# Kernel optimization log

Hardware: AMD Instinct MI355X
Metric: run time of the kernel (lower is better)

Reference implementation:

```python
import jax, jax.numpy as jnp
import numpy as np

NODE_F = 8      # node_features
HID = 128       # hidden_dim
HEADS = 8       # nn.MultiheadAttention num_heads
OUT = 256       # output_dim
MAX_ATOMS = 4096  # max_pocket_atoms
NEIGHBOR_RADIUS = 3.0   # _compute_surface_scores neighbor_radius


def setup_inputs() -> dict:
    key = jax.random.key(0)
    ks = jax.random.split(key, 16)
    N, M = 16384, 32
    x = jax.random.normal(ks[0], (N, NODE_F), dtype=jnp.float32)
    pos = jax.random.normal(ks[1], (N, 3), dtype=jnp.float32) * 10.0
    ligand_pos = jax.random.normal(ks[2], (M, 3), dtype=jnp.float32) * 3.0

    def lin(k, fan_in, fan_out):
        return jax.random.normal(k, (fan_in, fan_out), dtype=jnp.float32) / np.sqrt(fan_in)

    return {
        'x': x, 'pos': pos, 'ligand_pos': ligand_pos,
        'W_node': lin(ks[3], NODE_F, HID), 'b_node': jnp.zeros((HID,), jnp.float32),
        'Wq': lin(ks[4], HID, HID), 'bq': jnp.zeros((HID,), jnp.float32),
        'Wk': lin(ks[5], HID, HID), 'bk': jnp.zeros((HID,), jnp.float32),
        'Wv': lin(ks[6], HID, HID), 'bv': jnp.zeros((HID,), jnp.float32),
        'Wo': lin(ks[7], HID, HID), 'bo': jnp.zeros((HID,), jnp.float32),
        'W1': lin(ks[8], HID, OUT), 'b1': jnp.zeros((OUT,), jnp.float32),
        'W2': lin(ks[9], OUT, OUT), 'b2': jnp.zeros((OUT,), jnp.float32),
    }


def _select_binding_site(pos, ligand_pos, k):
    # select_by_binding_site_proximity: distance-to-ligand-center + surface scores, topk
    lig_center = jnp.mean(ligand_pos, axis=0)                       # [3]
    d_lig = jnp.linalg.norm(pos - lig_center, axis=1)               # [N]
    # _compute_surface_scores: cdist(pos,pos) < 3.0, count neighbors (minus self)
    sq = jnp.sum(pos * pos, axis=1)                                 # [N]
    d2 = sq[:, None] + sq[None, :] - 2.0 * (pos @ pos.T)            # [N,N] squared distances
    neighbor_counts = jnp.sum(d2 < NEIGHBOR_RADIUS ** 2, axis=1) - 1
    surface = 1.0 / (neighbor_counts.astype(jnp.float32) + 1.0)
    scores = 1.0 / (1.0 + d_lig / 5.0) + 0.5 * surface
    _, idx = jax.lax.top_k(scores, k)                               # largest=True
    return idx


def reference(x, pos, ligand_pos, W_node, b_node, Wq, bq, Wk, bk, Wv, bv, Wo, bo, W1, b1, W2, b2):
    # N > max_pocket_atoms -> smart selection (adaptive with ligand_pos => binding_site)
    idx = _select_binding_site(pos, ligand_pos, MAX_ATOMS)
    xs = x[idx]                                                     # [K, NODE_F]

    # node embedding (E3 net call fails in the original -> h = node_embedding(x))
    h = xs @ W_node + b_node                                        # [K, HID]

    # MultiheadAttention over the single (batch=None) sequence, eval mode (no dropout)
    K = MAX_ATOMS
    dh = HID // HEADS
    q = (h @ Wq + bq).reshape(K, HEADS, dh).transpose(1, 0, 2)      # [H,K,dh]
    k_ = (h @ Wk + bk).reshape(K, HEADS, dh).transpose(1, 0, 2)
    v = (h @ Wv + bv).reshape(K, HEADS, dh).transpose(1, 0, 2)
    attn = jax.nn.softmax(jnp.einsum('hqd,hkd->hqk', q, k_) / np.sqrt(dh), axis=-1)
    av = jnp.einsum('hqk,hkd->hqd', attn, v).transpose(1, 0, 2).reshape(K, HID)
    h_att = av @ Wo + bo                                            # [K, HID]

    # global mean pool + output projection (Linear-ReLU-Linear)
    pooled = jnp.mean(h_att, axis=0)                                # [HID]
    out = jax.nn.relu(pooled @ W1 + b1) @ W2 + b2                   # [OUT]
    return out
```

## Files before the change

### kernel.cpp

```cpp
#include <hip/hip_runtime.h>
#include <cstdint>
#include <cstddef>

#define NPTS 16384
#define KSEL 4096
#define HIDDEN 128
#define NHEADS 8
#define DHEAD 16
#define OUTD 256
#define NSLICE 4
#define FCAP 262144
#define LCAP 2048
#define TAU 0.15f
#define HROW 264

typedef __attribute__((ext_vector_type(8))) short bf16x8;
typedef __attribute__((ext_vector_type(4))) float f32x4;
typedef __attribute__((ext_vector_type(16))) float f32x16;

#if defined(__has_builtin)
#if __has_builtin(__builtin_amdgcn_exp2f)
#define E2(x) __builtin_amdgcn_exp2f(x)
#endif
#endif
#ifndef E2
#define E2(x) exp2f(x)
#endif

constexpr size_t OFF_PA    = 1024;
constexpr size_t OFF_PB    = OFF_PA  + (size_t)NPTS*32;
constexpr size_t OFF_SQ    = OFF_PB  + (size_t)NPTS*32;
constexpr size_t OFF_DL    = OFF_SQ  + (size_t)NPTS*4;
constexpr size_t OFF_CNT   = OFF_DL  + (size_t)NPTS*4;
constexpr size_t OFF_NFLAG = OFF_CNT + (size_t)NPTS*4;
constexpr size_t OFF_FLG   = OFF_NFLAG + 1024;
constexpr size_t OFF_SEL   = OFF_FLG + (size_t)FCAP*4;
constexpr size_t SZ_PK     = (size_t)NHEADS*KSEL*32*2;
constexpr size_t OFF_QPK   = OFF_SEL + (size_t)KSEL*4;
constexpr size_t OFF_KPK   = OFF_QPK + SZ_PK;
constexpr size_t OFF_V     = OFF_KPK + SZ_PK;
constexpr size_t OFF_LP    = OFF_V  + (size_t)KSEL*HIDDEN*4;
constexpr size_t OFF_WP    = OFF_LP + (size_t)NHEADS*KSEL*NSLICE*4;
constexpr size_t OFF_PAV   = OFF_WP + (size_t)NHEADS*KSEL*NSLICE*4;
constexpr size_t OFF_WSP   = OFF_PAV + 1024;

__device__ __forceinline__ unsigned short f2bf(float f) {
    union { float f; unsigned u; } v; v.f = f;
    unsigned r = v.u + 0x7fffu + ((v.u >> 16) & 1u);
    return (unsigned short)(r >> 16);
}
__device__ __forceinline__ float bf2f(unsigned short h) {
    union { unsigned u; float f; } v; v.u = ((unsigned)h) << 16;
    return v.f;
}

__global__ void __launch_bounds__(256) k_prep(const float* __restrict__ pos, const float* __restrict__ lig, int M,
                       unsigned short* __restrict__ pa, unsigned short* __restrict__ pb,
                       float* __restrict__ sq, float* __restrict__ dl,
                       int* __restrict__ cnt, unsigned int* __restrict__ nflag, float* __restrict__ pav) {
    __shared__ float ls[128];
    __shared__ float ctr[3];
    int tid = threadIdx.x;
    int i = blockIdx.x * 256 + tid;
    cnt[i] = 0;
    if (i == 0) *nflag = 0;
    if (blockIdx.x == 0 && tid < HIDDEN) pav[tid] = 0.f;
    for (int k = tid; k < 3 * M; k += 256) ls[k] = lig[k];
    __syncthreads();
    if (tid < 3) {
        float s = 0.f;
        for (int k = 0; k < M; k++) s += ls[k * 3 + tid];
        ctr[tid] = s / (float)M;
    }
    __syncthreads();
    float x = pos[i*3+0], y = pos[i*3+1], z = pos[i*3+2];
    float s = (x*x + y*y) + z*z;
    sq[i] = s;
    float dx = x - ctr[0], dy = y - ctr[1], dz = z - ctr[2];
    dl[i] = sqrtf((dx*dx + dy*dy) + dz*dz);
    unsigned short xh = f2bf(x); float xr = bf2f(xh); float xl = x - xr;
    unsigned short yh = f2bf(y); float yr = bf2f(yh); float yl = y - yr;
    unsigned short zh = f2bf(z); float zr = bf2f(zh); float zl = z - zr;
    unsigned short xlb = f2bf(xl), ylb = f2bf(yl), zlb = f2bf(zl);
    unsigned short xhA = f2bf(-2.f*xr), xlA = f2bf(-2.f*xl);
    unsigned short yhA = f2bf(-2.f*yr), ylA = f2bf(-2.f*yl);
    unsigned short zhA = f2bf(-2.f*zr), zlA = f2bf(-2.f*zl);
    unsigned short sih = f2bf(s);
    unsigned short sil = f2bf(s - bf2f(sih));
    unsigned short one = f2bf(1.0f);
    union { unsigned short s[16]; float4 f[2]; } A, B;
    A.s[0]=xhA; A.s[1]=xhA; A.s[2]=xlA;
    A.s[3]=yhA; A.s[4]=yhA; A.s[5]=ylA;
    A.s[6]=zhA; A.s[7]=zhA; A.s[8]=zlA;
    A.s[9]=xlA; A.s[10]=ylA; A.s[11]=zlA;
    A.s[12]=sih; A.s[13]=sil; A.s[14]=one; A.s[15]=one;
    B.s[0]=xh;  B.s[1]=xlb;  B.s[2]=xh;
    B.s[3]=yh;  B.s[4]=ylb;  B.s[5]=yh;
    B.s[6]=zh;  B.s[7]=zlb;  B.s[8]=zh;
    B.s[9]=xlb; B.s[10]=ylb; B.s[11]=zlb;
    B.s[12]=one; B.s[13]=one; B.s[14]=sih; B.s[15]=sil;
    float4* pad = (float4*)(pa + (size_t)i * 16);
    pad[0] = A.f[0]; pad[1] = A.f[1];
    float4* pbd = (float4*)(pb + (size_t)i * 16);
    pbd[0] = B.f[0]; pbd[1] = B.f[1];
}

__global__ void __launch_bounds__(256) k_wsplit(const float* __restrict__ Wq, const float* __restrict__ Wk,
                                                const float* __restrict__ Wv, unsigned short* __restrict__ wsp) {
    const float* W = (blockIdx.x == 0) ? Wq : ((blockIdx.x == 1) ? Wk : Wv);
    unsigned short* dst = wsp + (size_t)blockIdx.x * HIDDEN * 256;
    for (int idx = threadIdx.x; idx < HIDDEN * HIDDEN; idx += 256) {
        int k = idx >> 7, n = idx & 127;
        float w = W[k * HIDDEN + n];
        unsigned short hi = f2bf(w);
        unsigned short lo = f2bf(w - bf2f(hi));
        dst[(size_t)n * 256 + k] = hi;
        dst[(size_t)n * 256 + 128 + k] = lo;
    }
}

__global__ void __launch_bounds__(256) k_neighbor(
        const unsigned short* __restrict__ pa, const unsigned short* __restrict__ pb,
        int* __restrict__ cnt, unsigned int* __restrict__ flg, unsigned int* __restrict__ nflag) {
    __shared__ unsigned short js[256 * 24];
    __shared__ unsigned int fbuf[LCAP];
    __shared__ unsigned int fcnt, fbase;
    int tid = threadIdx.x;
    if (tid == 0) fcnt = 0;
    int lane = tid & 63, w = tid >> 6;
    int half = lane >> 5, il = lane & 31;
    int i = blockIdx.x * 128 + w * 32 + il;
    bf16x8 bfrag = *(const bf16x8*)(pb + (size_t)i * 16 + half * 8);
    int jb0 = blockIdx.y * 1024;
    int acc = 0;
    for (int chv = 0; chv < 4; chv++) {
        int jb = jb0 + chv * 256;
        __syncthreads();
        {
            const float4* src = (const float4*)(pa + (size_t)(jb + tid) * 16);
            float4 v0 = src[0], v1 = src[1];
            float4* dst = (float4*)&js[tid * 24];
            dst[0] = v0; dst[1] = v1;
        }
        __syncthreads();
        #pragma unroll 2
        for (int t = 0; t < 8; t++) {
            bf16x8 afrag = *(const bf16x8*)&js[(t * 32 + il) * 24 + half * 8];
            f32x16 c = {0.f,0.f,0.f,0.f,0.f,0.f,0.f,0.f,0.f,0.f,0.f,0.f,0.f,0.f,0.f,0.f};
            c = __builtin_amdgcn_mfma_f32_32x32x16_bf16(afrag, bfrag, c, 0, 0, 0);
            int cs = 0, cl = 0;
            #pragma unroll
            for (int r = 0; r < 16; r++) {
                cs += (c[r] < 9.0f - TAU);
                cl += (c[r] < 9.0f + TAU);
            }
            if (cl == cs) {
                acc += cs;
            } else {
                unsigned jt9 = (unsigned)((jb >> 5) + t);
                unsigned xx = atomicAdd(&fcnt, 1u);
                if (xx < LCAP) fbuf[xx] = ((unsigned)i << 10) | (jt9 << 1) | (unsigned)half;
            }
        }
    }
    acc += __shfl_xor(acc, 32);
    if (half == 0) atomicAdd(&cnt[i], acc);
    __syncthreads();
    if (tid == 0) {
        unsigned cf = fcnt; if (cf > LCAP) cf = LCAP;
        fcnt = cf;
        fbase = atomicAdd(nflag, cf);
    }
    __syncthreads();
    unsigned cf = fcnt, fb = fbase;
    for (unsigned xx = tid; xx < cf; xx += 256) {
        unsigned di = fb + xx;
        if (di < FCAP) flg[di] = fbuf[xx];
    }
}

__global__ void __launch_bounds__(256) k_fixup(const float* __restrict__ pos, const float* __restrict__ sq,
        const unsigned int* __restrict__ flg, const unsigned int* __restrict__ nflag,
        int* __restrict__ cnt) {
    int nf = (int)*nflag; if (nf > FCAP) nf = FCAP;
    for (int idx = blockIdx.x * 256 + threadIdx.x; idx < nf; idx += gridDim.x * 256) {
        unsigned pr = flg[idx];
        int i = (int)(pr >> 10);
        int jt = (int)((pr >> 1) & 511u) << 5;
        int half = (int)(pr & 1u);
        float xi = pos[i*3+0], yi = pos[i*3+1], zi = pos[i*3+2];
        float si = sq[i];
        int add = 0;
        #pragma unroll
        for (int r = 0; r < 16; r++) {
            int j = jt + (r & 3) + 8 * (r >> 2) + 4 * half;
            float xj = pos[j*3+0], yj = pos[j*3+1], zj = pos[j*3+2];
            float dot = fmaf(xi, xj, fmaf(yi, yj, zi * zj));
            float d2 = (si + sq[j]) - 2.0f * dot;
            add += (d2 < 9.0f);
        }
        atomicAdd(&cnt[i], add);
    }
}

__global__ void __launch_bounds__(1024) k_select(const float* __restrict__ dl, const int* __restrict__ cnt,
                                                 int* __restrict__ sel) {
    __shared__ unsigned int sk[NPTS];
    __shared__ int hist[256];
    __shared__ int scan2[256];
    __shared__ unsigned int s_prefix;
    __shared__ int s_rem, s_eqtot, s_nout, s_digit, s_cgt;
    int tid = threadIdx.x;
    for (int i = tid; i < NPTS; i += 1024) {
        float score = 1.0f / (1.0f + dl[i] / 5.0f) + 0.5f * (1.0f / (float)cnt[i]);
        unsigned int u = __float_as_uint(score);
        sk[i] = u ^ ((u & 0x80000000u) ? 0xFFFFFFFFu : 0x80000000u);
    }
    if (tid == 0) { s_prefix = 0; s_rem = KSEL; s_nout = 0; s_eqtot = 0; }
    __syncthreads();
    for (int p = 0; p < 4; p++) {
        int sh = 24 - 8 * p;
        if (tid < 256) hist[tid] = 0;
        __syncthreads();
        unsigned int pref = s_prefix;
        int shp = (p == 0) ? 0 : (32 - 8 * p);
        for (int i = tid; i < NPTS; i += 1024) {
            unsigned int key = sk[i];
            bool m = (p == 0) || ((key >> shp) == pref);
            if (m) atomicAdd(&hist[(key >> sh) & 255], 1);
        }
        __syncthreads();
        if (tid < 256) scan2[tid] = hist[tid];
        __syncthreads();
        for (int off = 1; off < 256; off <<= 1) {
            int v = 0;
            if (tid < 256) { v = scan2[tid]; if (tid + off < 256) v += scan2[tid + off]; }
            __syncthreads();
            if (tid < 256) scan2[tid] = v;
            __syncthreads();
        }
        int rem = s_rem;
        if (tid < 256) {
            int hi = scan2[tid];
            int lo = hi - hist[tid];
            if (hi >= rem && lo < rem) { s_digit = tid; s_cgt = lo; }
        }
        __syncthreads();
        if (tid == 0) {
            s_prefix = (s_prefix << 8) | (unsigned int)s_digit;
            s_rem = rem - s_cgt;
            if (p == 3) s_eqtot = hist[s_digit];
        }
        __syncthreads();
    }
    unsigned int T = s_prefix;
    int need_eq = s_rem;
    for (int i = tid; i < NPTS; i += 1024)
        if (sk[i] > T) sel[atomicAdd(&s_nout, 1)] = i;
    __syncthreads();
    if (s_eqtot == need_eq) {
        for (int i = tid; i < NPTS; i += 1024)
            if (sk[i] == T) sel[atomicAdd(&s_nout, 1)] = i;
    } else {
        for (int i = tid; i < NPTS; i += 1024) {
            if (sk[i] == T) {
                int rank = 0;
                for (int j = 0; j < i; j++) rank += (sk[j] == T);
                if (rank < need_eq) sel[atomicAdd(&s_nout, 1)] = i;
            }
        }
    }
}

__global__ void __launch_bounds__(256) k_qkv(const float* __restrict__ x, const int* __restrict__ sel,
        const float* __restrict__ Wn, const float* __restrict__ bn,
        const float* __restrict__ bq, const float* __restrict__ bk, const float* __restrict__ bv,
        const unsigned short* __restrict__ wsp,
        unsigned short* __restrict__ qpk, unsigned short* __restrict__ kpk,
        float* __restrict__ vg) {
    __shared__ float xs[32][8];
    __shared__ unsigned short hsp[32 * HROW];
    int tid = threadIdx.x;
    int r0 = blockIdx.x * 32;
    int proj = blockIdx.y;
    { int rr = tid >> 3, cc = tid & 7; xs[rr][cc] = x[(size_t)sel[r0 + rr] * 8 + cc]; }
    __syncthreads();
    {
        int d = tid & 127, rp = tid >> 7;
        float wn[8];
        #pragma unroll
        for (int c = 0; c < 8; c++) wn[c] = Wn[c * HIDDEN + d];
        float b = bn[d];
        for (int r = rp; r < 32; r += 2) {
            float a = b;
            #pragma unroll
            for (int c = 0; c < 8; c++) a = fmaf(xs[r][c], wn[c], a);
            unsigned short hi = f2bf(a);
            unsigned short lo = f2bf(a - bf2f(hi));
            hsp[r * HROW + d] = hi;
            hsp[r * HROW + 128 + d] = lo;
        }
    }
    __syncthreads();
    int lane = tid & 63, w = tid >> 6;
    int n = lane & 15, g = lane >> 4;
    int rloc = (w & 1) * 16;
    int chalf = w >> 1;
    const unsigned short* wb = wsp + (size_t)proj * HIDDEN * 256;
    const unsigned short* arow = &hsp[(rloc + n) * HROW + ((g < 2) ? 0 : 128) + (g & 1) * 8];
    int b1off = (g & 1) * 8;
    for (int tc = 0; tc < 4; tc++) {
        int col0 = chalf * 64 + tc * 16;
        const unsigned short* bcol = wb + (size_t)(col0 + n) * 256;
        f32x4 acc = {0.f, 0.f, 0.f, 0.f};
        #pragma unroll
        for (int c = 0; c < 8; c++) {
            bf16x8 af = *(const bf16x8*)(arow + c * 16);
            bf16x8 b1 = *(const bf16x8*)(bcol + c * 16 + b1off);
            bf16x8 b2 = {0,0,0,0,0,0,0,0};
            if (g < 2) b2 = *(const bf16x8*)(bcol + 128 + c * 16 + b1off);
            acc = __builtin_amdgcn_mfma_f32_16x16x32_bf16(af, b1, acc, 0, 0, 0);
            acc = __builtin_amdgcn_mfma_f32_16x16x32_bf16(af, b2, acc, 0, 0, 0);
        }
        int col = col0 + n;
        int hh = col >> 4, dd = col & 15;
        if (proj == 0) {
            float bb = bq[col];
            #pragma unroll
            for (int r = 0; r < 4; r++) {
                int qrow = r0 + rloc + g * 4 + r;
                float val = (acc[r] + bb) * 0.36067376022224085f;
                unsigned short hi = f2bf(val);
                unsigned short lo = f2bf(val - bf2f(hi));
                size_t idx = ((size_t)(hh * KSEL) + qrow) * 32 + dd;
                qpk[idx] = hi; qpk[idx + 16] = lo;
            }
        } else if (proj == 1) {
            float bb = bk[col];
            #pragma unroll
            for (int r = 0; r < 4; r++) {
                int qrow = r0 + rloc + g * 4 + r;
                float val = acc[r] + bb;
                unsigned short hi = f2bf(val);
                unsigned short lo = f2bf(val - bf2f(hi));
                size_t idx = ((size_t)(hh * KSEL) + qrow) * 32 + dd;
                kpk[idx] = hi; kpk[idx + 16] = lo;
            }
        } else {
            float bb = bv[col];
            #pragma unroll
            for (int r = 0; r < 4; r++) {
                int qrow = r0 + rloc + g * 4 + r;
                vg[(size_t)qrow * HIDDEN + col] = acc[r] + bb;
            }
        }
    }
}

__global__ void __launch_bounds__(256) k_attn_l(
        const unsigned short* __restrict__ qpk, const unsigned short* __restrict__ kpk,
        float* __restrict__ lp) {
    __shared__ unsigned short smem[256 * 40];
    int tid = threadIdx.x;
    int ks = blockIdx.x, yg = blockIdx.y, h = blockIdx.z;
    size_t hb = (size_t)h * KSEL;
    int lane = tid & 63, w = tid >> 6;
    int n = lane & 15, g = lane >> 4;
    int q0w = yg * 64 + w * 16;
    bf16x8 afrag = *(const bf16x8*)(qpk + (hb + q0w + n) * 32 + g * 8);
    float l0 = 0.f, l1 = 0.f, l2 = 0.f, l3 = 0.f;
    int b1off = (g & 1) * 8;
    int b2off = 16 + g * 8;
    for (int kc = 0; kc < 4; kc++) {
        __syncthreads();
        {
            int krow = ks * 1024 + kc * 256 + tid;
            const float4* src = (const float4*)(kpk + (hb + krow) * 32);
            float4 a0 = src[0], a1 = src[1], a2 = src[2], a3 = src[3];
            float4* dst = (float4*)&smem[tid * 40];
            dst[0] = a0; dst[1] = a1; dst[2] = a2; dst[3] = a3;
        }
        __syncthreads();
        #pragma unroll 4
        for (int t = 0; t < 16; t++) {
            const unsigned short* rowp = &smem[(t * 16 + n) * 40];
            bf16x8 b1 = *(const bf16x8*)(rowp + b1off);
            bf16x8 b2 = {0,0,0,0,0,0,0,0};
            if (g < 2) b2 = *(const bf16x8*)(rowp + b2off);
            f32x4 c = {0.f, 0.f, 0.f, 0.f};
            c = __builtin_amdgcn_mfma_f32_16x16x32_bf16(afrag, b1, c, 0, 0, 0);
            c = __builtin_amdgcn_mfma_f32_16x16x32_bf16(afrag, b2, c, 0, 0, 0);
            l0 += E2(c[0]); l1 += E2(c[1]); l2 += E2(c[2]); l3 += E2(c[3]);
        }
    }
    #pragma unroll
    for (int m = 1; m < 16; m <<= 1) {
        l0 += __shfl_xor(l0, m); l1 += __shfl_xor(l1, m);
        l2 += __shfl_xor(l2, m); l3 += __shfl_xor(l3, m);
    }
    if (n == 0) {
        size_t base = (hb + q0w + g * 4) * NSLICE + ks;
        lp[base]            = l0; lp[base + NSLICE]     = l1;
        lp[base + 2*NSLICE] = l2; lp[base + 3*NSLICE]   = l3;
    }
}

__global__ void __launch_bounds__(256) k_attn_w(
        const unsigned short* __restrict__ qpk, const unsigned short* __restrict__ kpk,
        const float* __restrict__ lp, float* __restrict__ wp) {
    __shared__ unsigned short smem[256 * 40];
    __shared__ float rls[256];
    int tid = threadIdx.x;
    int qs = blockIdx.x, yg = blockIdx.y, h = blockIdx.z;
    size_t hb = (size_t)h * KSEL;
    int lane = tid & 63, w = tid >> 6;
    int n = lane & 15, g = lane >> 4;
    int j0w = yg * 64 + w * 16;
    bf16x8 afrag = *(const bf16x8*)(kpk + (hb + j0w + n) * 32 + g * 8);
    float w0 = 0.f, w1 = 0.f, w2 = 0.f, w3 = 0.f;
    int b1off = (g & 1) * 8;
    int b2off = 16 + g * 8;
    for (int qc = 0; qc < 4; qc++) {
        __syncthreads();
        {
            int qrow = qs * 1024 + qc * 256 + tid;
            const float4* src = (const float4*)(qpk + (hb + qrow) * 32);
            float4 a0 = src[0], a1 = src[1], a2 = src[2], a3 = src[3];
            float4* dst = (float4*)&smem[tid * 40];
            dst[0] = a0; dst[1] = a1; dst[2] = a2; dst[3] = a3;
            float4 p = ((const float4*)lp)[hb + qrow];
            rls[tid] = 1.0f / ((p.x + p.y) + (p.z + p.w));
        }
        __syncthreads();
        #pragma unroll 4
        for (int t = 0; t < 16; t++) {
            const unsigned short* rowp = &smem[(t * 16 + n) * 40];
            bf16x8 b1 = *(const bf16x8*)(rowp + b1off);
            bf16x8 b2 = {0,0,0,0,0,0,0,0};
            if (g < 2) b2 = *(const bf16x8*)(rowp + b2off);
            f32x4 c = {0.f, 0.f, 0.f, 0.f};
            c = __builtin_amdgcn_mfma_f32_16x16x32_bf16(afrag, b1, c, 0, 0, 0);
            c = __builtin_amdgcn_mfma_f32_16x16x32_bf16(afrag, b2, c, 0, 0, 0);
            float rv = rls[t * 16 + n];
            w0 = fmaf(E2(c[0]), rv, w0); w1 = fmaf(E2(c[1]), rv, w1);
            w2 = fmaf(E2(c[2]), rv, w2); w3 = fmaf(E2(c[3]), rv, w3);
        }
    }
    #pragma unroll
    for (int m = 1; m < 16; m <<= 1) {
        w0 += __shfl_xor(w0, m); w1 += __shfl_xor(w1, m);
        w2 += __shfl_xor(w2, m); w3 += __shfl_xor(w3, m);
    }
    if (n == 0) {
        size_t base = (hb + j0w + g * 4) * NSLICE + qs;
        wp[base]            = w0; wp[base + NSLICE]     = w1;
        wp[base + 2*NSLICE] = w2; wp[base + 3*NSLICE]   = w3;
    }
}

__global__ void __launch_bounds__(256) k_colsum(const float* __restrict__ wp, const float* __restrict__ vg,
                                                float* __restrict__ pav) {
    __shared__ float wl[NHEADS][32];
    __shared__ float red[128];
    int tid = threadIdx.x;
    int j0 = blockIdx.x * 32;
    {
        int h = tid >> 5, jl = tid & 31;
        float4 p = ((const float4*)wp)[(size_t)h * KSEL + j0 + jl];
        wl[h][jl] = (p.x + p.y) + (p.z + p.w);
    }
    __syncthreads();
    int d = tid & 127, g = tid >> 7;
    int h = d >> 4;
    float acc = 0.f;
    for (int jl = g * 16; jl < g * 16 + 16; jl++)
        acc = fmaf(wl[h][jl], vg[(size_t)(j0 + jl) * HIDDEN + d], acc);
    if (g == 1) red[d] = acc;
    __syncthreads();
    if (g == 0) atomicAdd(&pav[d], (acc + red[d]) * (1.0f / (float)KSEL));
}

__global__ void __launch_bounds__(256) k_final(const float* __restrict__ pav,
        const float* __restrict__ Wo, const float* __restrict__ bo,
        const float* __restrict__ W1, const float* __restrict__ b1,
        const float* __restrict__ W2, const float* __restrict__ b2,
        float* __restrict__ out) {
    __shared__ float sp[HIDDEN];
    __shared__ float st[OUTD];
    int t = threadIdx.x;
    if (t < HIDDEN) {
        float a = bo[t];
        for (int c = 0; c < HIDDEN; c++) a = fmaf(pav[c], Wo[c * HIDDEN + t], a);
        sp[t] = a;
    }
    __syncthreads();
    {
        float a = b1[t];
        for (int c = 0; c < HIDDEN; c++) a = fmaf(sp[c], W1[c * OUTD + t], a);
        st[t] = fmaxf(a, 0.f);
    }
    __syncthreads();
    {
        float o = b2[t];
        for (int c = 0; c < OUTD; c++) o = fmaf(st[c], W2[c * OUTD + t], o);
        out[t] = o;
    }
}

extern "C" void kernel_launch(void* const* d_in, const int* in_sizes, int n_in,
                              void* d_out, int out_size, void* d_ws, size_t ws_size,
                              hipStream_t stream) {
    (void)n_in; (void)out_size; (void)ws_size;
    const float* x   = (const float*)d_in[0];
    const float* pos = (const float*)d_in[1];
    const float* lig = (const float*)d_in[2];
    const float* Wn  = (const float*)d_in[3];
    const float* bn  = (const float*)d_in[4];
    const float* Wq  = (const float*)d_in[5];
    const float* bq  = (const float*)d_in[6];
    const float* Wk  = (const float*)d_in[7];
    const float* bk  = (const float*)d_in[8];
    const float* Wv  = (const float*)d_in[9];
    const float* bv  = (const float*)d_in[10];
    const float* Wo  = (const float*)d_in[11];
    const float* bo  = (const float*)d_in[12];
    const float* W1  = (const float*)d_in[13];
    const float* b1  = (const float*)d_in[14];
    const float* W2  = (const float*)d_in[15];
    const float* b2  = (const float*)d_in[16];
    int M = in_sizes[2] / 3;

    char* ws = (char*)d_ws;
    unsigned short* pa  = (unsigned short*)(ws + OFF_PA);
    unsigned short* pb  = (unsigned short*)(ws + OFF_PB);
    float*          sq  = (float*)(ws + OFF_SQ);
    float*          dl  = (float*)(ws + OFF_DL);
    int*            cnt = (int*)  (ws + OFF_CNT);
    unsigned int*   nfl = (unsigned int*)(ws + OFF_NFLAG);
    unsigned int*   flg = (unsigned int*)(ws + OFF_FLG);
    int*            sel = (int*)  (ws + OFF_SEL);
    unsigned short* qpk = (unsigned short*)(ws + OFF_QPK);
    unsigned short* kpk = (unsigned short*)(ws + OFF_KPK);
    float*          vg  = (float*)(ws + OFF_V);
    float*          lp  = (float*)(ws + OFF_LP);
    float*          wp  = (float*)(ws + OFF_WP);
    float*          pav = (float*)(ws + OFF_PAV);
    unsigned short* wsp = (unsigned short*)(ws + OFF_WSP);

    hipLaunchKernelGGL(k_prep,     dim3(64),       dim3(256),  0, stream, pos, lig, M, pa, pb, sq, dl, cnt, nfl, pav);
    hipLaunchKernelGGL(k_wsplit,   dim3(3),        dim3(256),  0, stream, Wq, Wk, Wv, wsp);
    hipLaunchKernelGGL(k_neighbor, dim3(128, 16),  dim3(256),  0, stream, pa, pb, cnt, flg, nfl);
    hipLaunchKernelGGL(k_fixup,    dim3(128),      dim3(256),  0, stream, pos, sq, flg, nfl, cnt);
    hipLaunchKernelGGL(k_select,   dim3(1),        dim3(1024), 0, stream, dl, cnt, sel);
    hipLaunchKernelGGL(k_qkv,      dim3(128, 3),   dim3(256),  0, stream, x, sel, Wn, bn, bq, bk, bv, wsp, qpk, kpk, vg);
    hipLaunchKernelGGL(k_attn_l,   dim3(4, 64, 8), dim3(256),  0, stream, qpk, kpk, lp);
    hipLaunchKernelGGL(k_attn_w,   dim3(4, 64, 8), dim3(256),  0, stream, qpk, kpk, lp, wp);
    hipLaunchKernelGGL(k_colsum,   dim3(KSEL/32),  dim3(256),  0, stream, wp, vg, pav);
    hipLaunchKernelGGL(k_final,    dim3(1),        dim3(256),  0, stream, pav, Wo, bo, W1, b1, W2, b2, (float*)d_out);
}
```

Before: 288.1 us.

## Use 32x32 MFMA tiles in attention kernels and fold weight split into prep

Both attention passes (softmax denominator and column-weight) switch from 16x16x32 MFMA tiles to 32x32x16 tiles, with each wave covering 32 rows. The three-term split-bf16 product (hi*hi + lo*hi + hi*lo) is computed explicitly, so the zero-padded fragment of the old layout goes away, the MFMA count per score drops and the grid is halved. The weight hi/lo split kernel is merged into k_prep as three extra blocks, removing one launch. In exchange each thread keeps 16 accumulators, which raises register pressure, and the cross-lane reductions and scattered stores grow.

Result: faster. 276.1 us (-4.2%).

```diff
diff --git a/kernel.cpp b/kernel.cpp
--- a/kernel.cpp
+++ b/kernel.cpp
@@ -57,10 +57,26 @@
 __global__ void __launch_bounds__(256) k_prep(const float* __restrict__ pos, const float* __restrict__ lig, int M,
                        unsigned short* __restrict__ pa, unsigned short* __restrict__ pb,
                        float* __restrict__ sq, float* __restrict__ dl,
-                       int* __restrict__ cnt, unsigned int* __restrict__ nflag, float* __restrict__ pav) {
+                       int* __restrict__ cnt, unsigned int* __restrict__ nflag, float* __restrict__ pav,
+                       const float* __restrict__ Wq, const float* __restrict__ Wk, const float* __restrict__ Wv,
+                       unsigned short* __restrict__ wsp) {
     __shared__ float ls[128];
     __shared__ float ctr[3];
     int tid = threadIdx.x;
+    if (blockIdx.x >= 64) {
+        int proj = blockIdx.x - 64;
+        const float* W = (proj == 0) ? Wq : ((proj == 1) ? Wk : Wv);
+        unsigned short* dst = wsp + (size_t)proj * HIDDEN * 256;
+        for (int idx = tid; idx < HIDDEN * HIDDEN; idx += 256) {
+            int k = idx >> 7, n = idx & 127;
+            float w = W[k * HIDDEN + n];
+            unsigned short hi = f2bf(w);
+            unsigned short lo = f2bf(w - bf2f(hi));
+            dst[(size_t)n * 256 + k] = hi;
+            dst[(size_t)n * 256 + 128 + k] = lo;
+        }
+        return;
+    }
     int i = blockIdx.x * 256 + tid;
     cnt[i] = 0;
     if (i == 0) *nflag = 0;
@@ -105,20 +121,6 @@
     pbd[0] = B.f[0]; pbd[1] = B.f[1];
 }
 
-__global__ void __launch_bounds__(256) k_wsplit(const float* __restrict__ Wq, const float* __restrict__ Wk,
-                                                const float* __restrict__ Wv, unsigned short* __restrict__ wsp) {
-    const float* W = (blockIdx.x == 0) ? Wq : ((blockIdx.x == 1) ? Wk : Wv);
-    unsigned short* dst = wsp + (size_t)blockIdx.x * HIDDEN * 256;
-    for (int idx = threadIdx.x; idx < HIDDEN * HIDDEN; idx += 256) {
-        int k = idx >> 7, n = idx & 127;
-        float w = W[k * HIDDEN + n];
-        unsigned short hi = f2bf(w);
-        unsigned short lo = f2bf(w - bf2f(hi));
-        dst[(size_t)n * 256 + k] = hi;
-        dst[(size_t)n * 256 + 128 + k] = lo;
-    }
-}
-
 __global__ void __launch_bounds__(256) k_neighbor(
         const unsigned short* __restrict__ pa, const unsigned short* __restrict__ pb,
         int* __restrict__ cnt, unsigned int* __restrict__ flg, unsigned int* __restrict__ nflag) {
@@ -365,12 +367,14 @@
     int ks = blockIdx.x, yg = blockIdx.y, h = blockIdx.z;
     size_t hb = (size_t)h * KSEL;
     int lane = tid & 63, w = tid >> 6;
-    int n = lane & 15, g = lane >> 4;
-    int q0w = yg * 64 + w * 16;
-    bf16x8 afrag = *(const bf16x8*)(qpk + (hb + q0w + n) * 32 + g * 8);
-    float l0 = 0.f, l1 = 0.f, l2 = 0.f, l3 = 0.f;
-    int b1off = (g & 1) * 8;
-    int b2off = 16 + g * 8;
+    int n = lane & 31, half = lane >> 5;
+    int q0 = yg * 128 + w * 32;
+    const unsigned short* qrow = qpk + (hb + q0 + n) * 32;
+    bf16x8 aQh = *(const bf16x8*)(qrow + half * 8);
+    bf16x8 aQl = *(const bf16x8*)(qrow + 16 + half * 8);
+    float lacc[16];
+    #pragma unroll
+    for (int r = 0; r < 16; r++) lacc[r] = 0.f;
     for (int kc = 0; kc < 4; kc++) {
         __syncthreads();
         {
@@ -381,27 +385,30 @@
             dst[0] = a0; dst[1] = a1; dst[2] = a2; dst[3] = a3;
         }
         __syncthreads();
-        #pragma unroll 4
-        for (int t = 0; t < 16; t++) {
-            const unsigned short* rowp = &smem[(t * 16 + n) * 40];
-            bf16x8 b1 = *(const bf16x8*)(rowp + b1off);
-            bf16x8 b2 = {0,0,0,0,0,0,0,0};
-            if (g < 2) b2 = *(const bf16x8*)(rowp + b2off);
-            f32x4 c = {0.f, 0.f, 0.f, 0.f};
-            c = __builtin_amdgcn_mfma_f32_16x16x32_bf16(afrag, b1, c, 0, 0, 0);
-            c = __builtin_amdgcn_mfma_f32_16x16x32_bf16(afrag, b2, c, 0, 0, 0);
-            l0 += E2(c[0]); l1 += E2(c[1]); l2 += E2(c[2]); l3 += E2(c[3]);
+        #pragma unroll 2
+        for (int t = 0; t < 8; t++) {
+            const unsigned short* rowp = &smem[(t * 32 + n) * 40];
+            bf16x8 bKh = *(const bf16x8*)(rowp + half * 8);
+            bf16x8 bKl = *(const bf16x8*)(rowp + 16 + half * 8);
+            f32x16 c = {0.f,0.f,0.f,0.f,0.f,0.f,0.f,0.f,0.f,0.f,0.f,0.f,0.f,0.f,0.f,0.f};
+            c = __builtin_amdgcn_mfma_f32_32x32x16_bf16(aQh, bKh, c, 0, 0, 0);
+            c = __builtin_amdgcn_mfma_f32_32x32x16_bf16(aQl, bKh, c, 0, 0, 0);
+            c = __builtin_amdgcn_mfma_f32_32x32x16_bf16(aQh, bKl, c, 0, 0, 0);
+            #pragma unroll
+            for (int r = 0; r < 16; r++) lacc[r] += E2(c[r]);
         }
     }
     #pragma unroll
-    for (int m = 1; m < 16; m <<= 1) {
-        l0 += __shfl_xor(l0, m); l1 += __shfl_xor(l1, m);
-        l2 += __shfl_xor(l2, m); l3 += __shfl_xor(l3, m);
+    for (int m = 1; m < 32; m <<= 1) {
+        #pragma unroll
+        for (int r = 0; r < 16; r++) lacc[r] += __shfl_xor(lacc[r], m);
     }
     if (n == 0) {
-        size_t base = (hb + q0w + g * 4) * NSLICE + ks;
-        lp[base]            = l0; lp[base + NSLICE]     = l1;
-        lp[base + 2*NSLICE] = l2; lp[base + 3*NSLICE]   = l3;
+        #pragma unroll
+        for (int r = 0; r < 16; r++) {
+            int q = q0 + (r & 3) + 8 * (r >> 2) + 4 * half;
+            lp[(hb + q) * NSLICE + ks] = lacc[r];
+        }
     }
 }
 
@@ -414,12 +421,14 @@
     int qs = blockIdx.x, yg = blockIdx.y, h = blockIdx.z;
     size_t hb = (size_t)h * KSEL;
     int lane = tid & 63, w = tid >> 6;
-    int n = lane & 15, g = lane >> 4;
-    int j0w = yg * 64 + w * 16;
-    bf16x8 afrag = *(const bf16x8*)(kpk + (hb + j0w + n) * 32 + g * 8);
-    float w0 = 0.f, w1 = 0.f, w2 = 0.f, w3 = 0.f;
-    int b1off = (g & 1) * 8;
-    int b2off = 16 + g * 8;
+    int n = lane & 31, half = lane >> 5;
+    int j0 = yg * 128 + w * 32;
+    const unsigned short* krow = kpk + (hb + j0 + n) * 32;
+    bf16x8 aKh = *(const bf16x8*)(krow + half * 8);
+    bf16x8 aKl = *(const bf16x8*)(krow + 16 + half * 8);
+    float wacc[16];
+    #pragma unroll
+    for (int r = 0; r < 16; r++) wacc[r] = 0.f;
     for (int qc = 0; qc < 4; qc++) {
         __syncthreads();
         {
@@ -432,29 +441,31 @@
             rls[tid] = 1.0f / ((p.x + p.y) + (p.z + p.w));
         }
         __syncthreads();
-        #pragma unroll 4
-        for (int t = 0; t < 16; t++) {
-            const unsigned short* rowp = &smem[(t * 16 + n) * 40];
-            bf16x8 b1 = *(const bf16x8*)(rowp + b1off);
-            bf16x8 b2 = {0,0,0,0,0,0,0,0};
-            if (g < 2) b2 = *(const bf16x8*)(rowp + b2off);
-            f32x4 c = {0.f, 0.f, 0.f, 0.f};
-            c = __builtin_amdgcn_mfma_f32_16x16x32_bf16(afrag, b1, c, 0, 0, 0);
-            c = __builtin_amdgcn_mfma_f32_16x16x32_bf16(afrag, b2, c, 0, 0, 0);
-            float rv = rls[t * 16 + n];
-            w0 = fmaf(E2(c[0]), rv, w0); w1 = fmaf(E2(c[1]), rv, w1);
-            w2 = fmaf(E2(c[2]), rv, w2); w3 = fmaf(E2(c[3]), rv, w3);
+        #pragma unroll 2
+        for (int t = 0; t < 8; t++) {
+            const unsigned short* rowp = &smem[(t * 32 + n) * 40];
+            bf16x8 bQh = *(const bf16x8*)(rowp + half * 8);
+            bf16x8 bQl = *(const bf16x8*)(rowp + 16 + half * 8);
+            f32x16 c = {0.f,0.f,0.f,0.f,0.f,0.f,0.f,0.f,0.f,0.f,0.f,0.f,0.f,0.f,0.f,0.f};
+            c = __builtin_amdgcn_mfma_f32_32x32x16_bf16(aKh, bQh, c, 0, 0, 0);
+            c = __builtin_amdgcn_mfma_f32_32x32x16_bf16(aKl, bQh, c, 0, 0, 0);
+            c = __builtin_amdgcn_mfma_f32_32x32x16_bf16(aKh, bQl, c, 0, 0, 0);
+            float rv = rls[t * 32 + n];
+            #pragma unroll
+            for (int r = 0; r < 16; r++) wacc[r] = fmaf(E2(c[r]), rv, wacc[r]);
         }
     }
     #pragma unroll
-    for (int m = 1; m < 16; m <<= 1) {
-        w0 += __shfl_xor(w0, m); w1 += __shfl_xor(w1, m);
-        w2 += __shfl_xor(w2, m); w3 += __shfl_xor(w3, m);
+    for (int m = 1; m < 32; m <<= 1) {
+        #pragma unroll
+        for (int r = 0; r < 16; r++) wacc[r] += __shfl_xor(wacc[r], m);
     }
     if (n == 0) {
-        size_t base = (hb + j0w + g * 4) * NSLICE + qs;
-        wp[base]            = w0; wp[base + NSLICE]     = w1;
-        wp[base + 2*NSLICE] = w2; wp[base + 3*NSLICE]   = w3;
+        #pragma unroll
+        for (int r = 0; r < 16; r++) {
+            int j = j0 + (r & 3) + 8 * (r >> 2) + 4 * half;
+            wp[(hb + j) * NSLICE + qs] = wacc[r];
+        }
     }
 }
 
@@ -547,14 +558,13 @@
     float*          pav = (float*)(ws + OFF_PAV);
     unsigned short* wsp = (unsigned short*)(ws + OFF_WSP);
 
-    hipLaunchKernelGGL(k_prep,     dim3(64),       dim3(256),  0, stream, pos, lig, M, pa, pb, sq, dl, cnt, nfl, pav);
-    hipLaunchKernelGGL(k_wsplit,   dim3(3),        dim3(256),  0, stream, Wq, Wk, Wv, wsp);
+    hipLaunchKernelGGL(k_prep,     dim3(67),       dim3(256),  0, stream, pos, lig, M, pa, pb, sq, dl, cnt, nfl, pav, Wq, Wk, Wv, wsp);
     hipLaunchKernelGGL(k_neighbor, dim3(128, 16),  dim3(256),  0, stream, pa, pb, cnt, flg, nfl);
     hipLaunchKernelGGL(k_fixup,    dim3(128),      dim3(256),  0, stream, pos, sq, flg, nfl, cnt);
     hipLaunchKernelGGL(k_select,   dim3(1),        dim3(1024), 0, stream, dl, cnt, sel);
     hipLaunchKernelGGL(k_qkv,      dim3(128, 3),   dim3(256),  0, stream, x, sel, Wn, bn, bq, bk, bv, wsp, qpk, kpk, vg);
-    hipLaunchKernelGGL(k_attn_l,   dim3(4, 64, 8), dim3(256),  0, stream, qpk, kpk, lp);
-    hipLaunchKernelGGL(k_attn_w,   dim3(4, 64, 8), dim3(256),  0, stream, qpk, kpk, lp, wp);
+    hipLaunchKernelGGL(k_attn_l,   dim3(4, 32, 8), dim3(256),  0, stream, qpk, kpk, lp);
+    hipLaunchKernelGGL(k_attn_w,   dim3(4, 32, 8), dim3(256),  0, stream, qpk, kpk, lp, wp);
     hipLaunchKernelGGL(k_colsum,   dim3(KSEL/32),  dim3(256),  0, stream, wp, vg, pav);
     hipLaunchKernelGGL(k_final,    dim3(1),        dim3(256),  0, stream, pav, Wo, bo, W1, b1, W2, b2, (float*)d_out);
 }
```
